# Performance work log

Hardware: AMD Instinct MI355X
Metric: run time of the kernel (lower is better)

## Reference

```python
import jax, jax.numpy as jnp
import numpy as np

N = 100000
E = 1600000
IN_F = 256
OUT_F = 128
ALPHA = 0.2  # LeakyReLU negative slope


def setup_inputs() -> dict:
    key = jax.random.key(0)
    k_x, k_e, k_w, k_al, k_ar = jax.random.split(key, 5)
    x = jax.random.normal(k_x, (N, IN_F), dtype=jnp.float32)
    edge_index = jax.random.randint(k_e, (2, E), 0, N, dtype=jnp.int64)
    # xavier_uniform with gain=1.414
    gain = 1.414
    lim_w = gain * np.sqrt(6.0 / (IN_F + OUT_F))
    W = jax.random.uniform(k_w, (IN_F, OUT_F), dtype=jnp.float32, minval=-lim_w, maxval=lim_w)
    lim_a = gain * np.sqrt(6.0 / (OUT_F + 1))
    a_left = jax.random.uniform(k_al, (OUT_F, 1), dtype=jnp.float32, minval=-lim_a, maxval=lim_a)
    a_right = jax.random.uniform(k_ar, (OUT_F, 1), dtype=jnp.float32, minval=-lim_a, maxval=lim_a)
    return {"x": x, "edge_index": edge_index, "W": W, "a_left": a_left, "a_right": a_right}


def reference(x, edge_index, W, a_left, a_right):
    src = edge_index[0]  # destination of aggregation (rows of adj)
    dst = edge_index[1]  # neighbor being attended to
    Wh = x @ W                              # [N, out_f]
    e_left = (Wh @ a_left)[:, 0]            # [N]
    e_right = (Wh @ a_right)[:, 0]          # [N]
    e = e_left[src] + e_right[dst]          # [E]
    e = jnp.where(e > 0, e, ALPHA * e)      # LeakyReLU
    # segment softmax over edges grouped by src node
    e_max = jax.ops.segment_max(e, src, num_segments=N)          # [N]
    e_exp = jnp.exp(e - e_max[src])                               # [E]
    e_sum = jax.ops.segment_sum(e_exp, src, num_segments=N)       # [N]
    alpha = e_exp / (e_sum[src] + 1e-9)                           # [E]
    messages = alpha[:, None] * Wh[dst]                           # [E, out_f]
    output = jax.ops.segment_sum(messages, src, num_segments=N)   # [N, out_f]
    return jax.nn.relu(output)
```

## Files before the change

### kernel.cpp

```cpp
#include <hip/hip_runtime.h>
#include <cstdint>
#include <cstddef>

static constexpr int IN_F  = 256;
static constexpr int OUT_F = 128;
#define ALPHA_SLOPE 0.2f
#define NB 256
#define BUCK_SH 7
#define CAP 6144

typedef __attribute__((ext_vector_type(8))) short short8;
typedef __attribute__((ext_vector_type(4))) float f32x4;
union ABFrag { uint32_t u[4]; short8 v; };

__device__ __forceinline__ uint32_t pack_bf2(float lo, float hi) {
    uint32_t ul = __float_as_uint(lo), uh = __float_as_uint(hi);
    uint32_t rl = (ul + 0x7fffu + ((ul >> 16) & 1u)) >> 16;
    uint32_t rh = (uh + 0x7fffu + ((uh >> 16) & 1u)) & 0xffff0000u;
    return rl | rh;
}
__device__ __forceinline__ uint32_t cvtpk_bf2(float lo, float hi) {
    uint32_t r;
    asm("v_cvt_pk_bf16_f32 %0, %1, %2" : "=v"(r) : "v"(lo), "v"(hi));
    return r;
}
__device__ __forceinline__ float blo(uint32_t w) { return __uint_as_float(w << 16); }
__device__ __forceinline__ float bhi(uint32_t w) { return __uint_as_float(w & 0xffff0000u); }

#define RL_F(x, l) __uint_as_float(__builtin_amdgcn_readlane(__float_as_uint(x), (l)))
#define RL_I(x, l) __builtin_amdgcn_readlane((x), (l))

__device__ __forceinline__ int edge_at(const void* ei, int idx, int is64) {
    return is64 ? (int)((const long long*)ei)[idx] : ((const int*)ei)[idx];
}

__global__ void prep_kernel(const float* __restrict__ W, const float* __restrict__ aL,
                            const float* __restrict__ aR, const unsigned* __restrict__ ei_u32,
                            uint32_t* __restrict__ WtH,
                            float* __restrict__ waL, float* __restrict__ waR,
                            int* __restrict__ flag) {
    if (blockIdx.x == 65) {
        __shared__ int cnt;
        if (threadIdx.x == 0) cnt = 0;
        __syncthreads();
        int nz = 0;
        for (int i = threadIdx.x; i < 1024; i += blockDim.x)
            if (ei_u32[2 * i + 1] != 0u) nz++;
        if (nz) atomicAdd(&cnt, nz);
        __syncthreads();
        if (threadIdx.x == 0) *flag = (cnt == 0) ? 1 : 0;
        return;
    }
    if (blockIdx.x == 64) {
        int k = threadIdx.x;
        const float* wr = W + (size_t)k * OUT_F;
        float sl = 0.f, sr = 0.f;
        for (int j = 0; j < OUT_F; j++) {
            float wv = wr[j];
            sl = fmaf(wv, aL[j], sl);
            sr = fmaf(wv, aR[j], sr);
        }
        waL[k] = sl; waR[k] = sr;
        return;
    }
    int dd = blockIdx.x * 256 + threadIdx.x;
    int n  = dd >> 7;
    int kd = (dd & 127) ^ ((n & 7) << 2);
    int k  = kd * 2;
    WtH[dd] = pack_bf2(W[(size_t)k * OUT_F + n], W[(size_t)(k + 1) * OUT_F + n]);
}

__global__ __launch_bounds__(512) void gemm_kernel(
    const float* __restrict__ X, const uint32_t* __restrict__ WtH,
    const float* __restrict__ waL, const float* __restrict__ waR,
    uint32_t* __restrict__ Whh, float* __restrict__ el, float* __restrict__ er,
    int M)
{
    __shared__ uint32_t ldsW[16384];
    const int tid = threadIdx.x;
    const int w = tid >> 6, l = tid & 63;
    const int c = l & 15, kg = l >> 4;
    const int swz = (c & 7) << 2;

    {
        const uint4* src = (const uint4*)WtH;
        uint4* dst = (uint4*)ldsW;
#pragma unroll
        for (int i = 0; i < 8; i++)
            dst[tid + i * 512] = src[tid + i * 512];
    }

    const int bm = blockIdx.x * 128;
    const int myrow = w * 16 + c;
    const int grow = min(bm + myrow, M - 1);
    const bool rv = (bm + myrow) < M;
    const float* xp = X + (size_t)grow * IN_F + kg * 8;

    float4 xv[16];
#pragma unroll
    for (int ks = 0; ks < 8; ks++) {
        xv[2 * ks]     = *(const float4*)(xp + ks * 32);
        xv[2 * ks + 1] = *(const float4*)(xp + ks * 32 + 4);
    }

    f32x4 acc[8];
#pragma unroll
    for (int j = 0; j < 8; j++) acc[j] = (f32x4){0.f, 0.f, 0.f, 0.f};
    float sl = 0.f, sr = 0.f;

    __syncthreads();

#pragma unroll
    for (int ks = 0; ks < 8; ks++) {
        float4 xa = xv[2 * ks], xb = xv[2 * ks + 1];
        const float* wlp = waL + ks * 32 + kg * 8;
        const float* wrp = waR + ks * 32 + kg * 8;
        float4 l0 = *(const float4*)wlp, l1 = *(const float4*)(wlp + 4);
        float4 r0 = *(const float4*)wrp, r1 = *(const float4*)(wrp + 4);
        sl = fmaf(xa.x, l0.x, sl); sl = fmaf(xa.y, l0.y, sl);
        sl = fmaf(xa.z, l0.z, sl); sl = fmaf(xa.w, l0.w, sl);
        sl = fmaf(xb.x, l1.x, sl); sl = fmaf(xb.y, l1.y, sl);
        sl = fmaf(xb.z, l1.z, sl); sl = fmaf(xb.w, l1.w, sl);
        sr = fmaf(xa.x, r0.x, sr); sr = fmaf(xa.y, r0.y, sr);
        sr = fmaf(xa.z, r0.z, sr); sr = fmaf(xa.w, r0.w, sr);
        sr = fmaf(xb.x, r1.x, sr); sr = fmaf(xb.y, r1.y, sr);
        sr = fmaf(xb.z, r1.z, sr); sr = fmaf(xb.w, r1.w, sr);
        ABFrag a;
        a.u[0] = cvtpk_bf2(xa.x, xa.y); a.u[1] = cvtpk_bf2(xa.z, xa.w);
        a.u[2] = cvtpk_bf2(xb.x, xb.y); a.u[3] = cvtpk_bf2(xb.z, xb.w);
        const int kd = ks * 16 + kg * 4;
#pragma unroll
        for (int j = 0; j < 8; j++) {
            const int col = j * 16 + c;
            ABFrag b;
            *(uint4*)b.u = *(const uint4*)&ldsW[col * 128 + (kd ^ swz)];
            acc[j] = __builtin_amdgcn_mfma_f32_16x16x32_bf16(a.v, b.v, acc[j], 0, 0, 0);
        }
    }

    sl += __shfl_xor(sl, 16); sl += __shfl_xor(sl, 32);
    sr += __shfl_xor(sr, 16); sr += __shfl_xor(sr, 32);
    if (rv && kg == 0) { el[bm + myrow] = sl; er[bm + myrow] = sr; }

    __syncthreads();
    float* sc = (float*)ldsW + w * 2048;
#pragma unroll
    for (int j = 0; j < 8; j++)
#pragma unroll
        for (int r = 0; r < 4; r++)
            sc[(kg * 4 + r) * 128 + j * 16 + c] = acc[j][r];
    __syncthreads();
#pragma unroll
    for (int m = 0; m < 16; m++) {
        float2 p = *(const float2*)&sc[m * 128 + 2 * l];
        int orow = bm + w * 16 + m;
        if (orow < M) Whh[(size_t)orow * 64 + l] = cvtpk_bf2(p.x, p.y);
    }
}

__global__ __launch_bounds__(256) void hist_kernel(const void* ei, const int* flag,
                                                   int E, int nbuk, int* __restrict__ C) {
    __shared__ int h[800];
    for (int b = threadIdx.x; b < nbuk; b += 256) h[b] = 0;
    __syncthreads();
    int is64 = *flag;
    int chunk = (E + NB - 1) / NB;
    int start = blockIdx.x * chunk;
    int end = min(start + chunk, E);
    for (int i = start + threadIdx.x; i < end; i += 256) {
        int s = edge_at(ei, i, is64);
        atomicAdd(&h[s >> BUCK_SH], 1);
    }
    __syncthreads();
    for (int b = threadIdx.x; b < nbuk; b += 256)
        C[b * NB + blockIdx.x] = h[b];
}

__global__ __launch_bounds__(256) void scan1_kernel(const int* __restrict__ counts,
                                                    int* __restrict__ offsets,
                                                    int* __restrict__ partials, int N) {
    __shared__ int wt[4];
    int gid = blockIdx.x * 256 + threadIdx.x;
    const int lane = threadIdx.x & 63, wave = threadIdx.x >> 6;
    int c = (gid < N) ? counts[gid] : 0;
    int incl = c;
#pragma unroll
    for (int o = 1; o < 64; o <<= 1) {
        int v = __shfl_up(incl, o);
        if (lane >= o) incl += v;
    }
    if (lane == 63) wt[wave] = incl;
    __syncthreads();
    int woff = 0;
    for (int w = 0; w < wave; w++) woff += wt[w];
    if (gid < N) offsets[gid] = woff + incl - c;
    if (threadIdx.x == 0) partials[blockIdx.x] = wt[0] + wt[1] + wt[2] + wt[3];
}

__global__ __launch_bounds__(256) void scan2_kernel(int* data, int n) {
    __shared__ int wt[4];
    __shared__ int carry_s;
    if (threadIdx.x == 0) carry_s = 0;
    __syncthreads();
    const int lane = threadIdx.x & 63, wave = threadIdx.x >> 6;
    for (int base = 0; base < n; base += 256) {
        int i = base + threadIdx.x;
        int c = (i < n) ? data[i] : 0;
        int incl = c;
#pragma unroll
        for (int o = 1; o < 64; o <<= 1) {
            int v = __shfl_up(incl, o);
            if (lane >= o) incl += v;
        }
        if (lane == 63) wt[wave] = incl;
        __syncthreads();
        int woff = 0;
        for (int w = 0; w < wave; w++) woff += wt[w];
        int total = wt[0] + wt[1] + wt[2] + wt[3];
        int carry = carry_s;
        __syncthreads();
        if (i < n) data[i] = carry + woff + incl - c;
        if (threadIdx.x == 0) carry_s = carry + total;
        __syncthreads();
    }
}

__global__ __launch_bounds__(256) void scatter_kernel(const void* ei, const int* flag,
                                                      int E, int nbuk,
                                                      const int* __restrict__ Cx,
                                                      const int* __restrict__ T,
                                                      uint32_t* __restrict__ entries) {
    __shared__ int cur[800];
    for (int b = threadIdx.x; b < nbuk; b += 256) cur[b] = 0;
    __syncthreads();
    int is64 = *flag;
    int chunk = (E + NB - 1) / NB;
    int start = blockIdx.x * chunk;
    int end = min(start + chunk, E);
    for (int i = start + threadIdx.x; i < end; i += 256) {
        int s = edge_at(ei, i, is64);
        int d = edge_at(ei, E + i, is64);
        int b = s >> BUCK_SH;
        int pos = T[b] + Cx[b * NB + blockIdx.x] + atomicAdd(&cur[b], 1);
        entries[pos] = ((uint32_t)(s & 127) << 17) | (uint32_t)d;
    }
}

__global__ __launch_bounds__(256) void bucket_kernel(const uint32_t* __restrict__ entries,
                                                     const int* __restrict__ T,
                                                     int E, int N, int nbuk,
                                                     int* __restrict__ offsets,
                                                     int* __restrict__ edge_dst) {
    __shared__ uint32_t ent[CAP];
    __shared__ int outD[CAP];
    __shared__ int cnt[128], pre[128], cur[128];
    __shared__ int wt4[2];
    const int b = blockIdx.x;
    const int tid = threadIdx.x;
    const int base = T[b];
    const int cend = (b + 1 < nbuk) ? T[b + 1] : E;
    int count = cend - base;
    if (count > CAP) count = CAP;

    if (tid < 128) { cnt[tid] = 0; cur[tid] = 0; }
    __syncthreads();
    for (int k = tid; k < count; k += 256) {
        uint32_t e = entries[base + k];
        ent[k] = e;
        atomicAdd(&cnt[e >> 17], 1);
    }
    __syncthreads();
    {
        const int lane = tid & 63, w = tid >> 6;
        int c = (tid < 128) ? cnt[tid] : 0;
        int incl = c;
#pragma unroll
        for (int o = 1; o < 64; o <<= 1) {
            int v = __shfl_up(incl, o);
            if (lane >= o) incl += v;
        }
        if (w == 0 && lane == 63) wt4[0] = incl;
        __syncthreads();
        if (tid < 128) pre[tid] = ((w == 1) ? wt4[0] : 0) + incl - c;
        __syncthreads();
    }
    const int node0 = b << BUCK_SH;
    const int nnode = min(128, N - node0);
    if (tid < nnode) offsets[node0 + tid] = base + pre[tid];
    if (b == nbuk - 1 && tid == 0) offsets[N] = E;
    for (int k = tid; k < count; k += 256) {
        uint32_t e = ent[k];
        int sl = e >> 17;
        int p = pre[sl] + atomicAdd(&cur[sl], 1);
        outD[p] = (int)(e & 0x1FFFFu);
    }
    __syncthreads();
    for (int k = tid; k < count; k += 256)
        edge_dst[base + k] = outD[k];
}

__global__ __launch_bounds__(256) void node_kernel(const int* __restrict__ offsets,
                                                   const int* __restrict__ edge_dst,
                                                   const float* __restrict__ el,
                                                   const float* __restrict__ er,
                                                   const uint32_t* __restrict__ WhH,
                                                   float* __restrict__ out, int N) {
    int node = blockIdx.x * 4 + (threadIdx.x >> 6);
    int lane = threadIdx.x & 63;
    if (node >= N) return;
    int s0  = offsets[node];
    int deg = offsets[node + 1] - s0;
    float eli = el[node];

    if (deg <= 64) {
        int dj = 0;
        float e = -3.402823466e38f;
        if (lane < deg) {
            dj = edge_dst[s0 + lane];
            float t = eli + er[dj];
            e = t > 0.f ? t : ALPHA_SLOPE * t;
        }
        float m = e;
#pragma unroll
        for (int o = 32; o > 0; o >>= 1) m = fmaxf(m, __shfl_xor(m, o));
        float ex = (lane < deg) ? expf(e - m) : 0.f;
        float ssum = ex;
#pragma unroll
        for (int o = 32; o > 0; o >>= 1) ssum += __shfl_xor(ssum, o);
        float p = ex / (ssum + 1e-9f);

        const int g = lane >> 4, q = lane & 15;
        float a0 = 0.f, a1 = 0.f, a2 = 0.f, a3 = 0.f;
        float a4 = 0.f, a5 = 0.f, a6 = 0.f, a7 = 0.f;
        int rounds = (deg + 3) >> 2;
        int r = 0;
        for (; r + 2 <= rounds; r += 2) {
            int s0i = (r << 2) + g, s1i = s0i + 4;
            float p0 = __shfl(p, s0i), p1 = __shfl(p, s1i);
            int   e0 = __shfl(dj, s0i), e1 = __shfl(dj, s1i);
            uint4 w0 = *(const uint4*)&WhH[(size_t)e0 * 64 + q * 4];
            uint4 w1 = *(const uint4*)&WhH[(size_t)e1 * 64 + q * 4];
            a0 = fmaf(p0, blo(w0.x), a0); a1 = fmaf(p0, bhi(w0.x), a1);
            a2 = fmaf(p0, blo(w0.y), a2); a3 = fmaf(p0, bhi(w0.y), a3);
            a4 = fmaf(p0, blo(w0.z), a4); a5 = fmaf(p0, bhi(w0.z), a5);
            a6 = fmaf(p0, blo(w0.w), a6); a7 = fmaf(p0, bhi(w0.w), a7);
            a0 = fmaf(p1, blo(w1.x), a0); a1 = fmaf(p1, bhi(w1.x), a1);
            a2 = fmaf(p1, blo(w1.y), a2); a3 = fmaf(p1, bhi(w1.y), a3);
            a4 = fmaf(p1, blo(w1.z), a4); a5 = fmaf(p1, bhi(w1.z), a5);
            a6 = fmaf(p1, blo(w1.w), a6); a7 = fmaf(p1, bhi(w1.w), a7);
        }
        if (r < rounds) {
            int s0i = (r << 2) + g;
            float p0 = __shfl(p, s0i);
            int   e0 = __shfl(dj, s0i);
            uint4 w0 = *(const uint4*)&WhH[(size_t)e0 * 64 + q * 4];
            a0 = fmaf(p0, blo(w0.x), a0); a1 = fmaf(p0, bhi(w0.x), a1);
            a2 = fmaf(p0, blo(w0.y), a2); a3 = fmaf(p0, bhi(w0.y), a3);
            a4 = fmaf(p0, blo(w0.z), a4); a5 = fmaf(p0, bhi(w0.z), a5);
            a6 = fmaf(p0, blo(w0.w), a6); a7 = fmaf(p0, bhi(w0.w), a7);
        }
#pragma unroll
        for (int o = 16; o <= 32; o <<= 1) {
            a0 += __shfl_xor(a0, o); a1 += __shfl_xor(a1, o);
            a2 += __shfl_xor(a2, o); a3 += __shfl_xor(a3, o);
            a4 += __shfl_xor(a4, o); a5 += __shfl_xor(a5, o);
            a6 += __shfl_xor(a6, o); a7 += __shfl_xor(a7, o);
        }
        if (g == 0) {
            float4 o0 = make_float4(fmaxf(a0, 0.f), fmaxf(a1, 0.f),
                                    fmaxf(a2, 0.f), fmaxf(a3, 0.f));
            float4 o1 = make_float4(fmaxf(a4, 0.f), fmaxf(a5, 0.f),
                                    fmaxf(a6, 0.f), fmaxf(a7, 0.f));
            float* op = out + (size_t)node * OUT_F + q * 8;
            *(float4*)op = o0;
            *(float4*)(op + 4) = o1;
        }
        return;
    }

    float m = -3.402823466e38f;
    for (int j = lane; j < deg; j += 64) {
        float e = eli + er[edge_dst[s0 + j]];
        e = e > 0.f ? e : ALPHA_SLOPE * e;
        m = fmaxf(m, e);
    }
#pragma unroll
    for (int o = 32; o > 0; o >>= 1) m = fmaxf(m, __shfl_xor(m, o));

    float ssum = 0.f;
    for (int j = lane; j < deg; j += 64) {
        float e = eli + er[edge_dst[s0 + j]];
        e = e > 0.f ? e : ALPHA_SLOPE * e;
        ssum += expf(e - m);
    }
#pragma unroll
    for (int o = 32; o > 0; o >>= 1) ssum += __shfl_xor(ssum, o);
    float inv = 1.f / (ssum + 1e-9f);

    float acc0 = 0.f, acc1 = 0.f;
    for (int base = 0; base < deg; base += 64) {
        int j = base + lane;
        float p = 0.f;
        int d = 0;
        if (j < deg) {
            d = edge_dst[s0 + j];
            float e = eli + er[d];
            e = e > 0.f ? e : ALPHA_SLOPE * e;
            p = expf(e - m) * inv;
        }
        int cnt = min(64, deg - base);
        int t = 0;
        for (; t + 8 <= cnt; t += 8) {
            float b0 = RL_F(p, t + 0), b1 = RL_F(p, t + 1);
            float b2 = RL_F(p, t + 2), b3 = RL_F(p, t + 3);
            float b4 = RL_F(p, t + 4), b5 = RL_F(p, t + 5);
            float b6 = RL_F(p, t + 6), b7 = RL_F(p, t + 7);
            int   d0 = RL_I(d, t + 0), d1 = RL_I(d, t + 1);
            int   d2 = RL_I(d, t + 2), d3 = RL_I(d, t + 3);
            int   d4 = RL_I(d, t + 4), d5 = RL_I(d, t + 5);
            int   d6 = RL_I(d, t + 6), d7 = RL_I(d, t + 7);
            uint32_t w0 = WhH[(size_t)d0 * 64 + lane];
            uint32_t w1 = WhH[(size_t)d1 * 64 + lane];
            uint32_t w2 = WhH[(size_t)d2 * 64 + lane];
            uint32_t w3 = WhH[(size_t)d3 * 64 + lane];
            uint32_t w4 = WhH[(size_t)d4 * 64 + lane];
            uint32_t w5 = WhH[(size_t)d5 * 64 + lane];
            uint32_t w6 = WhH[(size_t)d6 * 64 + lane];
            uint32_t w7 = WhH[(size_t)d7 * 64 + lane];
            acc0 = fmaf(b0, blo(w0), acc0); acc1 = fmaf(b0, bhi(w0), acc1);
            acc0 = fmaf(b1, blo(w1), acc0); acc1 = fmaf(b1, bhi(w1), acc1);
            acc0 = fmaf(b2, blo(w2), acc0); acc1 = fmaf(b2, bhi(w2), acc1);
            acc0 = fmaf(b3, blo(w3), acc0); acc1 = fmaf(b3, bhi(w3), acc1);
            acc0 = fmaf(b4, blo(w4), acc0); acc1 = fmaf(b4, bhi(w4), acc1);
            acc0 = fmaf(b5, blo(w5), acc0); acc1 = fmaf(b5, bhi(w5), acc1);
            acc0 = fmaf(b6, blo(w6), acc0); acc1 = fmaf(b6, bhi(w6), acc1);
            acc0 = fmaf(b7, blo(w7), acc0); acc1 = fmaf(b7, bhi(w7), acc1);
        }
        for (; t < cnt; ++t) {
            float a = RL_F(p, t);
            int  dd = RL_I(d, t);
            uint32_t wv = WhH[(size_t)dd * 64 + lane];
            acc0 = fmaf(a, blo(wv), acc0);
            acc1 = fmaf(a, bhi(wv), acc1);
        }
    }
    out[(size_t)node * OUT_F + 2 * lane]     = fmaxf(acc0, 0.f);
    out[(size_t)node * OUT_F + 2 * lane + 1] = fmaxf(acc1, 0.f);
}

extern "C" void kernel_launch(void* const* d_in, const int* in_sizes, int n_in,
                              void* d_out, int out_size, void* d_ws, size_t ws_size,
                              hipStream_t stream) {
    (void)n_in; (void)out_size; (void)ws_size;
    const float* X  = (const float*)d_in[0];
    const void*  EI = d_in[1];
    const float* W  = (const float*)d_in[2];
    const float* aL = (const float*)d_in[3];
    const float* aR = (const float*)d_in[4];
    float* out = (float*)d_out;
    const int N = in_sizes[0] / IN_F;
    const int E = in_sizes[1] / 2;
    const int nbuk = (N + 127) >> BUCK_SH;

    char* ws = (char*)d_ws;
    int*      flag     = (int*)ws;
    float*    waL      = (float*)(ws + 256);
    float*    waR      = waL + 256;
    uint32_t* WtH      = (uint32_t*)(waR + 256);
    uint32_t* Whh      = WtH + 16384;
    float*    el       = (float*)(Whh + (size_t)N * 64);
    float*    er       = el + N;
    int*      T        = (int*)(er + N);
    int*      C        = T + 1024;
    int*      Cx       = C + (size_t)nbuk * NB;
    int*      offsets  = Cx + (size_t)nbuk * NB;
    uint32_t* entries  = (uint32_t*)(offsets + (N + 1));
    int*      edge_dst = (int*)(entries + E);

    prep_kernel<<<66, 256, 0, stream>>>(W, aL, aR, (const unsigned*)EI,
                                        WtH, waL, waR, flag);
    gemm_kernel<<<(N + 127) / 128, 512, 0, stream>>>(X, WtH, waL, waR, Whh, el, er, N);
    hist_kernel<<<NB, 256, 0, stream>>>(EI, flag, E, nbuk, C);
    scan1_kernel<<<nbuk, 256, 0, stream>>>(C, Cx, T, nbuk * NB);
    scan2_kernel<<<1, 256, 0, stream>>>(T, nbuk);
    scatter_kernel<<<NB, 256, 0, stream>>>(EI, flag, E, nbuk, Cx, T, entries);
    bucket_kernel<<<nbuk, 256, 0, stream>>>(entries, T, E, N, nbuk, offsets, edge_dst);
    node_kernel<<<(N + 3) / 4, 256, 0, stream>>>(offsets, edge_dst, el, er, Whh, out, N);
}
```

Before: 161.4 us.

## Merge prep with histogram and GEMM with scatter; unroll gather loop by four

Combines weight preparation and the edge histogram into one launch, and runs the GEMM blocks together with the edge scatter blocks in one grid, so the independent stages overlap and launch count drops from eight to six. Each histogram and scatter block now detects the int64 edge format itself, replacing the shared flag. Separately, the node aggregation loop is unrolled to four outstanding gathers per iteration. The costs are redundant format detection per block, extra LDS in the GEMM kernel for the scatter path, and higher register pressure in the node kernel.

```diff
diff --git a/kernel.cpp b/kernel.cpp
--- a/kernel.cpp
+++ b/kernel.cpp
@@ -34,21 +34,18 @@
     return is64 ? (int)((const long long*)ei)[idx] : ((const int*)ei)[idx];
 }
 
-__global__ void prep_kernel(const float* __restrict__ W, const float* __restrict__ aL,
-                            const float* __restrict__ aR, const unsigned* __restrict__ ei_u32,
-                            uint32_t* __restrict__ WtH,
-                            float* __restrict__ waL, float* __restrict__ waR,
-                            int* __restrict__ flag) {
-    if (blockIdx.x == 65) {
-        __shared__ int cnt;
-        if (threadIdx.x == 0) cnt = 0;
-        __syncthreads();
-        int nz = 0;
-        for (int i = threadIdx.x; i < 1024; i += blockDim.x)
-            if (ei_u32[2 * i + 1] != 0u) nz++;
-        if (nz) atomicAdd(&cnt, nz);
-        __syncthreads();
-        if (threadIdx.x == 0) *flag = (cnt == 0) ? 1 : 0;
+__global__ __launch_bounds__(256) void prep_hist_kernel(
+    const float* __restrict__ W, const float* __restrict__ aL,
+    const float* __restrict__ aR, const void* __restrict__ EI,
+    int E, int nbuk, uint32_t* __restrict__ WtH,
+    float* __restrict__ waL, float* __restrict__ waR, int* __restrict__ C)
+{
+    if (blockIdx.x < 64) {
+        int dd = blockIdx.x * 256 + threadIdx.x;
+        int n  = dd >> 7;
+        int kd = (dd & 127) ^ ((n & 7) << 2);
+        int k  = kd * 2;
+        WtH[dd] = pack_bf2(W[(size_t)k * OUT_F + n], W[(size_t)(k + 1) * OUT_F + n]);
         return;
     }
     if (blockIdx.x == 64) {
@@ -63,21 +60,122 @@
         waL[k] = sl; waR[k] = sr;
         return;
     }
-    int dd = blockIdx.x * 256 + threadIdx.x;
-    int n  = dd >> 7;
-    int kd = (dd & 127) ^ ((n & 7) << 2);
-    int k  = kd * 2;
-    WtH[dd] = pack_bf2(W[(size_t)k * OUT_F + n], W[(size_t)(k + 1) * OUT_F + n]);
-}
-
-__global__ __launch_bounds__(512) void gemm_kernel(
+    __shared__ int h[800];
+    __shared__ int det;
+    if (threadIdx.x == 0) det = 0;
+    for (int b = threadIdx.x; b < nbuk; b += 256) h[b] = 0;
+    __syncthreads();
+    {
+        const unsigned* eu = (const unsigned*)EI;
+        int nz = 0;
+        for (int i = threadIdx.x; i < 1024; i += 256)
+            if (eu[2 * i + 1] != 0u) nz++;
+        if (nz) atomicAdd(&det, 1);
+    }
+    __syncthreads();
+    const int is64 = (det == 0);
+    const int bid = blockIdx.x - 65;
+    int chunk = (E + NB - 1) / NB;
+    int start = bid * chunk;
+    int end = min(start + chunk, E);
+    for (int i = start + threadIdx.x; i < end; i += 256) {
+        int s = edge_at(EI, i, is64);
+        atomicAdd(&h[s >> BUCK_SH], 1);
+    }
+    __syncthreads();
+    for (int b = threadIdx.x; b < nbuk; b += 256)
+        C[b * NB + bid] = h[b];
+}
+
+__global__ __launch_bounds__(256) void scan1_kernel(const int* __restrict__ counts,
+                                                    int* __restrict__ offsets,
+                                                    int* __restrict__ partials, int N) {
+    __shared__ int wt[4];
+    int gid = blockIdx.x * 256 + threadIdx.x;
+    const int lane = threadIdx.x & 63, wave = threadIdx.x >> 6;
+    int c = (gid < N) ? counts[gid] : 0;
+    int incl = c;
+#pragma unroll
+    for (int o = 1; o < 64; o <<= 1) {
+        int v = __shfl_up(incl, o);
+        if (lane >= o) incl += v;
+    }
+    if (lane == 63) wt[wave] = incl;
+    __syncthreads();
+    int woff = 0;
+    for (int w = 0; w < wave; w++) woff += wt[w];
+    if (gid < N) offsets[gid] = woff + incl - c;
+    if (threadIdx.x == 0) partials[blockIdx.x] = wt[0] + wt[1] + wt[2] + wt[3];
+}
+
+__global__ __launch_bounds__(256) void scan2_kernel(int* data, int n) {
+    __shared__ int wt[4];
+    __shared__ int carry_s;
+    if (threadIdx.x == 0) carry_s = 0;
+    __syncthreads();
+    const int lane = threadIdx.x & 63, wave = threadIdx.x >> 6;
+    for (int base = 0; base < n; base += 256) {
+        int i = base + threadIdx.x;
+        int c = (i < n) ? data[i] : 0;
+        int incl = c;
+#pragma unroll
+        for (int o = 1; o < 64; o <<= 1) {
+            int v = __shfl_up(incl, o);
+            if (lane >= o) incl += v;
+        }
+        if (lane == 63) wt[wave] = incl;
+        __syncthreads();
+        int woff = 0;
+        for (int w = 0; w < wave; w++) woff += wt[w];
+        int total = wt[0] + wt[1] + wt[2] + wt[3];
+        int carry = carry_s;
+        __syncthreads();
+        if (i < n) data[i] = carry + woff + incl - c;
+        if (threadIdx.x == 0) carry_s = carry + total;
+        __syncthreads();
+    }
+}
+
+__global__ __launch_bounds__(512) void gemm_scatter_kernel(
     const float* __restrict__ X, const uint32_t* __restrict__ WtH,
     const float* __restrict__ waL, const float* __restrict__ waR,
     uint32_t* __restrict__ Whh, float* __restrict__ el, float* __restrict__ er,
-    int M)
+    int M, const void* __restrict__ EI, int E, int nbuk,
+    const int* __restrict__ Cx, const int* __restrict__ T,
+    uint32_t* __restrict__ entries, int GB)
 {
     __shared__ uint32_t ldsW[16384];
+    __shared__ int cur[800];
+    __shared__ int det;
     const int tid = threadIdx.x;
+
+    if (blockIdx.x >= GB) {
+        if (tid == 0) det = 0;
+        for (int b = tid; b < nbuk; b += 512) cur[b] = 0;
+        __syncthreads();
+        {
+            const unsigned* eu = (const unsigned*)EI;
+            int nz = 0;
+            for (int i = tid; i < 1024; i += 512)
+                if (eu[2 * i + 1] != 0u) nz++;
+            if (nz) atomicAdd(&det, 1);
+        }
+        __syncthreads();
+        const int is64 = (det == 0);
+        const int bid = blockIdx.x - GB;
+        int chunk = (E + NB - 1) / NB;
+        int start = bid * chunk;
+        int end = min(start + chunk, E);
+        for (int i = start + tid; i < end; i += 512) {
+            int s = edge_at(EI, i, is64);
+            int d = edge_at(EI, E + i, is64);
+            int b = s >> BUCK_SH;
+            int pos = T[b] + Cx[b * NB + bid] + atomicAdd(&cur[b], 1);
+            entries[pos] = ((uint32_t)(s & 127) << 17) | (uint32_t)d;
+        }
+        return;
+    }
+
     const int w = tid >> 6, l = tid & 63;
     const int c = l & 15, kg = l >> 4;
     const int swz = (c & 7) << 2;
@@ -158,94 +256,6 @@
     }
 }
 
-__global__ __launch_bounds__(256) void hist_kernel(const void* ei, const int* flag,
-                                                   int E, int nbuk, int* __restrict__ C) {
-    __shared__ int h[800];
-    for (int b = threadIdx.x; b < nbuk; b += 256) h[b] = 0;
-    __syncthreads();
-    int is64 = *flag;
-    int chunk = (E + NB - 1) / NB;
-    int start = blockIdx.x * chunk;
-    int end = min(start + chunk, E);
-    for (int i = start + threadIdx.x; i < end; i += 256) {
-        int s = edge_at(ei, i, is64);
-        atomicAdd(&h[s >> BUCK_SH], 1);
-    }
-    __syncthreads();
-    for (int b = threadIdx.x; b < nbuk; b += 256)
-        C[b * NB + blockIdx.x] = h[b];
-}
-
-__global__ __launch_bounds__(256) void scan1_kernel(const int* __restrict__ counts,
-                                                    int* __restrict__ offsets,
-                                                    int* __restrict__ partials, int N) {
-    __shared__ int wt[4];
-    int gid = blockIdx.x * 256 + threadIdx.x;
-    const int lane = threadIdx.x & 63, wave = threadIdx.x >> 6;
-    int c = (gid < N) ? counts[gid] : 0;
-    int incl = c;
-#pragma unroll
-    for (int o = 1; o < 64; o <<= 1) {
-        int v = __shfl_up(incl, o);
-        if (lane >= o) incl += v;
-    }
-    if (lane == 63) wt[wave] = incl;
-    __syncthreads();
-    int woff = 0;
-    for (int w = 0; w < wave; w++) woff += wt[w];
-    if (gid < N) offsets[gid] = woff + incl - c;
-    if (threadIdx.x == 0) partials[blockIdx.x] = wt[0] + wt[1] + wt[2] + wt[3];
-}
-
-__global__ __launch_bounds__(256) void scan2_kernel(int* data, int n) {
-    __shared__ int wt[4];
-    __shared__ int carry_s;
-    if (threadIdx.x == 0) carry_s = 0;
-    __syncthreads();
-    const int lane = threadIdx.x & 63, wave = threadIdx.x >> 6;
-    for (int base = 0; base < n; base += 256) {
-        int i = base + threadIdx.x;
-        int c = (i < n) ? data[i] : 0;
-        int incl = c;
-#pragma unroll
-        for (int o = 1; o < 64; o <<= 1) {
-            int v = __shfl_up(incl, o);
-            if (lane >= o) incl += v;
-        }
-        if (lane == 63) wt[wave] = incl;
-        __syncthreads();
-        int woff = 0;
-        for (int w = 0; w < wave; w++) woff += wt[w];
-        int total = wt[0] + wt[1] + wt[2] + wt[3];
-        int carry = carry_s;
-        __syncthreads();
-        if (i < n) data[i] = carry + woff + incl - c;
-        if (threadIdx.x == 0) carry_s = carry + total;
-        __syncthreads();
-    }
-}
-
-__global__ __launch_bounds__(256) void scatter_kernel(const void* ei, const int* flag,
-                                                      int E, int nbuk,
-                                                      const int* __restrict__ Cx,
-                                                      const int* __restrict__ T,
-                                                      uint32_t* __restrict__ entries) {
-    __shared__ int cur[800];
-    for (int b = threadIdx.x; b < nbuk; b += 256) cur[b] = 0;
-    __syncthreads();
-    int is64 = *flag;
-    int chunk = (E + NB - 1) / NB;
-    int start = blockIdx.x * chunk;
-    int end = min(start + chunk, E);
-    for (int i = start + threadIdx.x; i < end; i += 256) {
-        int s = edge_at(ei, i, is64);
-        int d = edge_at(ei, E + i, is64);
-        int b = s >> BUCK_SH;
-        int pos = T[b] + Cx[b * NB + blockIdx.x] + atomicAdd(&cur[b], 1);
-        entries[pos] = ((uint32_t)(s & 127) << 17) | (uint32_t)d;
-    }
-}
-
 __global__ __launch_bounds__(256) void bucket_kernel(const uint32_t* __restrict__ entries,
                                                      const int* __restrict__ T,
                                                      int E, int N, int nbuk,
@@ -334,10 +344,37 @@
         float a4 = 0.f, a5 = 0.f, a6 = 0.f, a7 = 0.f;
         int rounds = (deg + 3) >> 2;
         int r = 0;
+        for (; r + 4 <= rounds; r += 4) {
+            int i0 = (r << 2) + g, i1 = i0 + 4, i2 = i0 + 8, i3 = i0 + 12;
+            float p0 = __shfl(p, i0), p1 = __shfl(p, i1);
+            float p2 = __shfl(p, i2), p3 = __shfl(p, i3);
+            int   e0 = __shfl(dj, i0), e1 = __shfl(dj, i1);
+            int   e2 = __shfl(dj, i2), e3 = __shfl(dj, i3);
+            uint4 w0 = *(const uint4*)&WhH[(size_t)e0 * 64 + q * 4];
+            uint4 w1 = *(const uint4*)&WhH[(size_t)e1 * 64 + q * 4];
+            uint4 w2 = *(const uint4*)&WhH[(size_t)e2 * 64 + q * 4];
+            uint4 w3 = *(const uint4*)&WhH[(size_t)e3 * 64 + q * 4];
+            a0 = fmaf(p0, blo(w0.x), a0); a1 = fmaf(p0, bhi(w0.x), a1);
+            a2 = fmaf(p0, blo(w0.y), a2); a3 = fmaf(p0, bhi(w0.y), a3);
+            a4 = fmaf(p0, blo(w0.z), a4); a5 = fmaf(p0, bhi(w0.z), a5);
+            a6 = fmaf(p0, blo(w0.w), a6); a7 = fmaf(p0, bhi(w0.w), a7);
+            a0 = fmaf(p1, blo(w1.x), a0); a1 = fmaf(p1, bhi(w1.x), a1);
+            a2 = fmaf(p1, blo(w1.y), a2); a3 = fmaf(p1, bhi(w1.y), a3);
+            a4 = fmaf(p1, blo(w1.z), a4); a5 = fmaf(p1, bhi(w1.z), a5);
+            a6 = fmaf(p1, blo(w1.w), a6); a7 = fmaf(p1, bhi(w1.w), a7);
+            a0 = fmaf(p2, blo(w2.x), a0); a1 = fmaf(p2, bhi(w2.x), a1);
+            a2 = fmaf(p2, blo(w2.y), a2); a3 = fmaf(p2, bhi(w2.y), a3);
+            a4 = fmaf(p2, blo(w2.z), a4); a5 = fmaf(p2, bhi(w2.z), a5);
+            a6 = fmaf(p2, blo(w2.w), a6); a7 = fmaf(p2, bhi(w2.w), a7);
+            a0 = fmaf(p3, blo(w3.x), a0); a1 = fmaf(p3, bhi(w3.x), a1);
+            a2 = fmaf(p3, blo(w3.y), a2); a3 = fmaf(p3, bhi(w3.y), a3);
+            a4 = fmaf(p3, blo(w3.z), a4); a5 = fmaf(p3, bhi(w3.z), a5);
+            a6 = fmaf(p3, blo(w3.w), a6); a7 = fmaf(p3, bhi(w3.w), a7);
+        }
         for (; r + 2 <= rounds; r += 2) {
-            int s0i = (r << 2) + g, s1i = s0i + 4;
-            float p0 = __shfl(p, s0i), p1 = __shfl(p, s1i);
-            int   e0 = __shfl(dj, s0i), e1 = __shfl(dj, s1i);
+            int i0 = (r << 2) + g, i1 = i0 + 4;
+            float p0 = __shfl(p, i0), p1 = __shfl(p, i1);
+            int   e0 = __shfl(dj, i0), e1 = __shfl(dj, i1);
             uint4 w0 = *(const uint4*)&WhH[(size_t)e0 * 64 + q * 4];
             uint4 w1 = *(const uint4*)&WhH[(size_t)e1 * 64 + q * 4];
             a0 = fmaf(p0, blo(w0.x), a0); a1 = fmaf(p0, bhi(w0.x), a1);
@@ -350,9 +387,9 @@
             a6 = fmaf(p1, blo(w1.w), a6); a7 = fmaf(p1, bhi(w1.w), a7);
         }
         if (r < rounds) {
-            int s0i = (r << 2) + g;
-            float p0 = __shfl(p, s0i);
-            int   e0 = __shfl(dj, s0i);
+            int i0 = (r << 2) + g;
+            float p0 = __shfl(p, i0);
+            int   e0 = __shfl(dj, i0);
             uint4 w0 = *(const uint4*)&WhH[(size_t)e0 * 64 + q * 4];
             a0 = fmaf(p0, blo(w0.x), a0); a1 = fmaf(p0, bhi(w0.x), a1);
             a2 = fmaf(p0, blo(w0.y), a2); a3 = fmaf(p0, bhi(w0.y), a3);
@@ -461,9 +498,9 @@
     const int N = in_sizes[0] / IN_F;
     const int E = in_sizes[1] / 2;
     const int nbuk = (N + 127) >> BUCK_SH;
+    const int GB = (N + 127) / 128;
 
     char* ws = (char*)d_ws;
-    int*      flag     = (int*)ws;
     float*    waL      = (float*)(ws + 256);
     float*    waR      = waL + 256;
     uint32_t* WtH      = (uint32_t*)(waR + 256);
@@ -477,13 +514,13 @@
     uint32_t* entries  = (uint32_t*)(offsets + (N + 1));
     int*      edge_dst = (int*)(entries + E);
 
-    prep_kernel<<<66, 256, 0, stream>>>(W, aL, aR, (const unsigned*)EI,
-                                        WtH, waL, waR, flag);
-    gemm_kernel<<<(N + 127) / 128, 512, 0, stream>>>(X, WtH, waL, waR, Whh, el, er, N);
-    hist_kernel<<<NB, 256, 0, stream>>>(EI, flag, E, nbuk, C);
+    prep_hist_kernel<<<65 + NB, 256, 0, stream>>>(W, aL, aR, EI, E, nbuk,
+                                                  WtH, waL, waR, C);
     scan1_kernel<<<nbuk, 256, 0, stream>>>(C, Cx, T, nbuk * NB);
     scan2_kernel<<<1, 256, 0, stream>>>(T, nbuk);
-    scatter_kernel<<<NB, 256, 0, stream>>>(EI, flag, E, nbuk, Cx, T, entries);
+    gemm_scatter_kernel<<<GB + NB, 512, 0, stream>>>(X, WtH, waL, waR, Whh, el, er,
+                                                     N, EI, E, nbuk, Cx, T,
+                                                     entries, GB);
     bucket_kernel<<<nbuk, 256, 0, stream>>>(entries, T, E, N, nbuk, offsets, edge_dst);
     node_kernel<<<(N + 3) / 4, 256, 0, stream>>>(offsets, edge_dst, el, er, Whh, out, N);
 }
```

Result: no change. 159.4 us (-1.3%).
